# Optimization experiments

Measured on AMD Instinct MI355X. Metric: run time of the kernel, lower is better.

Reference implementation:

```python
import jax, jax.numpy as jnp
import numpy as np

VOL = (256, 256, 256)
K = 64  # number of connected components (clusters)


def setup_inputs() -> dict:
    key = jax.random.key(0)
    k1, k2, k3 = jax.random.split(key, 3)
    # Precomputed connected-component labels of (pred + target) > 0.
    # 0 = background, 1..K = clusters.
    labels = jax.random.randint(k1, VOL, 0, K + 1, dtype=jnp.int32)
    fg = labels > 0
    # Binary prediction / ground-truth masks, nonzero only inside labeled regions
    # (consistent with labels being components of the overlay of pred and target).
    pred = ((jax.random.uniform(k2, VOL) < 0.6) & fg).astype(jnp.float32)
    target = ((jax.random.uniform(k3, VOL) < 0.6) & fg).astype(jnp.float32)
    return {"pred": pred, "target": target, "labels": labels, "num_clusters": K}


def reference(pred, target, labels, num_clusters):
    # Per-cluster dice via one fused segment reduction instead of a Python loop
    # over clusters. Segment 0 is background and is dropped, matching
    # range(1, num_features + 1) in the original.
    lab = labels.reshape(-1)
    p = pred.reshape(-1)
    t = target.reshape(-1)
    nseg = num_clusters + 1
    # intersection = sum(pred_cluster * gt_cluster); pred/target are binary so
    # logical_and(...).float() products reduce to pred * target per segment.
    inter = jax.ops.segment_sum(p * t, lab, num_segments=nseg)[1:]
    sum_p = jax.ops.segment_sum(p, lab, num_segments=nseg)[1:]
    sum_t = jax.ops.segment_sum(t, lab, num_segments=nseg)[1:]
    union = sum_p + sum_t
    dice = jnp.where(union > 0, 2.0 * inter / jnp.maximum(union, 1.0), 1.0)
    return 1.0 - jnp.mean(dice)
```

## Files before the change

kernel.cpp:

```cpp
#include <hip/hip_runtime.h>


#define NSEG 65
#define NREP 64
#define REP_MASK 63
#define NCOPY 16
#define BLOCKS 4096
#define THREADS 256
#define GP 4

__device__ __forceinline__ unsigned int pack32(float p, float t) {
    unsigned int sp = (p != 0.0f) ? 1u : 0u;
    unsigned int st = (t != 0.0f) ? 1u : 0u;
    return ((sp & st) << 20) | (sp << 10) | st;
}

__device__ __forceinline__ void accum4(unsigned int (*s_cnt)[NSEG], int copy,
                                       float4 p, float4 t, int4 l) {
    atomicAdd(&s_cnt[copy][l.x], pack32(p.x, t.x));
    atomicAdd(&s_cnt[copy][l.y], pack32(p.y, t.y));
    atomicAdd(&s_cnt[copy][l.z], pack32(p.z, t.z));
    atomicAdd(&s_cnt[copy][l.w], pack32(p.w, t.w));
}

__global__ __launch_bounds__(THREADS, 8) void seg_count_kernel(
    const float* __restrict__ pred,
    const float* __restrict__ target,
    const int* __restrict__ labels,
    unsigned long long* __restrict__ part,
    int n)
{
    __shared__ unsigned int s_cnt[NCOPY][NSEG];
    const int tid = threadIdx.x;
    const int copy = tid >> 4;
    const int rep = (int)blockIdx.x & REP_MASK;

    for (int i = tid; i < NCOPY * NSEG; i += THREADS)
        ((unsigned int*)s_cnt)[i] = 0u;
    __syncthreads();

    const int n_vec = n >> 2;
    const float4* __restrict__ p4 = (const float4*)pred;
    const float4* __restrict__ t4 = (const float4*)target;
    const int4*   __restrict__ l4 = (const int4*)labels;

    const int chunk = (n_vec + (int)gridDim.x - 1) / (int)gridDim.x;
    const int base = blockIdx.x * chunk;
    const int end = min(base + chunk, n_vec);

    if (end - base == GP * THREADS) {
        int idx = base + tid;
        float4 pa = p4[idx];
        float4 ta = t4[idx];
        int4   la = l4[idx];
        #pragma unroll
        for (int g = 1; g < GP; ++g) {
            float4 pb = p4[idx + g * THREADS];
            float4 tb = t4[idx + g * THREADS];
            int4   lb = l4[idx + g * THREADS];
            accum4(s_cnt, copy, pa, ta, la);
            pa = pb; ta = tb; la = lb;
        }
        accum4(s_cnt, copy, pa, ta, la);
    } else {
        for (int idx = base + tid; idx < end; idx += THREADS)
            accum4(s_cnt, copy, p4[idx], t4[idx], l4[idx]);
    }

    if (blockIdx.x == 0) {
        for (int i = (n_vec << 2) + tid; i < n; i += THREADS)
            atomicAdd(&s_cnt[copy][labels[i]], pack32(pred[i], target[i]));
    }
    __syncthreads();

    for (int s = tid; s < NSEG; s += THREADS) {
        unsigned long long in = 0, sp = 0, st = 0;
        #pragma unroll
        for (int c = 0; c < NCOPY; ++c) {
            unsigned int v = s_cnt[c][s];
            st += v & 0x3FFu;
            sp += (v >> 10) & 0x3FFu;
            in += v >> 20;
        }
        unsigned long long tot = (in << 42) | (sp << 21) | st;
        if (tot) atomicAdd(&part[s * NREP + rep], tot);
    }
}

__global__ __launch_bounds__(256) void dice_finalize_kernel(
    const unsigned long long* __restrict__ part,
    const int* __restrict__ nc_ptr,
    float* __restrict__ out)
{
    const int nc = *nc_ptr;
    const int tid = threadIdx.x;
    const int s = 1 + (tid >> 2);
    const int q = tid & 3;

    unsigned long long acc = 0;
    const unsigned long long* row = part + s * NREP + q * 16;
    #pragma unroll
    for (int i = 0; i < 16; ++i) acc += row[i];
    acc += __shfl_xor(acc, 1);
    acc += __shfl_xor(acc, 2);

    __shared__ float s_dice[64];
    if (q == 0) {
        float in = (float)(acc >> 42);
        float sp = (float)((acc >> 21) & 0x1FFFFFull);
        float st = (float)(acc & 0x1FFFFFull);
        float uni = sp + st;
        float dice = (uni > 0.0f) ? (2.0f * in / uni) : 1.0f;
        s_dice[s - 1] = (s <= nc) ? dice : 0.0f;
    }
    __syncthreads();

    if (tid < 64) {
        float local = s_dice[tid];
        #pragma unroll
        for (int off = 32; off > 0; off >>= 1)
            local += __shfl_down(local, off);
        if (tid == 0) out[0] = 1.0f - local / (float)nc;
    }
}

extern "C" void kernel_launch(void* const* d_in, const int* in_sizes, int n_in,
                              void* d_out, int out_size, void* d_ws, size_t ws_size,
                              hipStream_t stream) {
    const float* pred   = (const float*)d_in[0];
    const float* target = (const float*)d_in[1];
    const int*   labels = (const int*)d_in[2];
    const int*   nc_ptr = (const int*)d_in[3];
    float* out = (float*)d_out;
    unsigned long long* part = (unsigned long long*)d_ws;

    const int n = in_sizes[0];

    hipMemsetAsync(d_ws, 0, NSEG * NREP * sizeof(unsigned long long), stream);

    seg_count_kernel<<<BLOCKS, THREADS, 0, stream>>>(
        pred, target, labels, part, n);
    dice_finalize_kernel<<<1, 256, 0, stream>>>(part, nc_ptr, out);
}
```

Baseline: 200.5 us.

## Software-pipeline loads with inline asm and staggered vmcnt waits, halve grid

Halves the grid and doubles the per-block work to eight float4 groups per thread. The compiler-scheduled loads are replaced with hand-written global_load_dwordx4 asm and explicit s_waitcnt vmcnt counters, so several loads of labels, target and pred stay in flight while LDS atomics run on earlier data. This is meant to hide memory latency better, at the cost of more registers and a lower occupancy hint. The hand-managed wait counts depend on exact issue order and rely on the compiler not inserting other vector-memory ops in between.

New measurement: 200.3 us. No clear change (-0.1%).

```diff
diff --git a/kernel.cpp b/kernel.cpp
--- a/kernel.cpp
+++ b/kernel.cpp
@@ -5,9 +5,21 @@
 #define NREP 64
 #define REP_MASK 63
 #define NCOPY 16
-#define BLOCKS 4096
+#define BLOCKS 2048
 #define THREADS 256
-#define GP 4
+#define GP 8
+
+typedef float4 f4;
+typedef int4 i4;
+
+#define GLOAD(dst, voff, base) \
+    asm volatile("global_load_dwordx4 %0, %1, %2" \
+                 : "=v"(dst) : "v"(voff), "s"(base))
+
+#define WAITN(NSTR) do { \
+    asm volatile("s_waitcnt vmcnt(" NSTR ")" ::: "memory"); \
+    __builtin_amdgcn_sched_barrier(0); \
+} while (0)
 
 __device__ __forceinline__ unsigned int pack32(float p, float t) {
     unsigned int sp = (p != 0.0f) ? 1u : 0u;
@@ -16,14 +28,14 @@
 }
 
 __device__ __forceinline__ void accum4(unsigned int (*s_cnt)[NSEG], int copy,
-                                       float4 p, float4 t, int4 l) {
+                                       f4 p, f4 t, i4 l) {
     atomicAdd(&s_cnt[copy][l.x], pack32(p.x, t.x));
     atomicAdd(&s_cnt[copy][l.y], pack32(p.y, t.y));
     atomicAdd(&s_cnt[copy][l.z], pack32(p.z, t.z));
     atomicAdd(&s_cnt[copy][l.w], pack32(p.w, t.w));
 }
 
-__global__ __launch_bounds__(THREADS, 8) void seg_count_kernel(
+__global__ __launch_bounds__(THREADS, 4) void seg_count_kernel(
     const float* __restrict__ pred,
     const float* __restrict__ target,
     const int* __restrict__ labels,
@@ -40,29 +52,53 @@
     __syncthreads();
 
     const int n_vec = n >> 2;
-    const float4* __restrict__ p4 = (const float4*)pred;
-    const float4* __restrict__ t4 = (const float4*)target;
-    const int4*   __restrict__ l4 = (const int4*)labels;
-
     const int chunk = (n_vec + (int)gridDim.x - 1) / (int)gridDim.x;
     const int base = blockIdx.x * chunk;
     const int end = min(base + chunk, n_vec);
 
     if (end - base == GP * THREADS) {
-        int idx = base + tid;
-        float4 pa = p4[idx];
-        float4 ta = t4[idx];
-        int4   la = l4[idx];
-        #pragma unroll
-        for (int g = 1; g < GP; ++g) {
-            float4 pb = p4[idx + g * THREADS];
-            float4 tb = t4[idx + g * THREADS];
-            int4   lb = l4[idx + g * THREADS];
-            accum4(s_cnt, copy, pa, ta, la);
-            pa = pb; ta = tb; la = lb;
-        }
-        accum4(s_cnt, copy, pa, ta, la);
+        const unsigned int vb = (unsigned int)(base + tid) * 16u;
+        f4 PA, PB;
+        f4 TA, TB, TC;
+        i4 LA, LB, LC, LD;
+
+        GLOAD(LA, vb,           labels);
+        GLOAD(LB, vb + 4096u,   labels);
+        GLOAD(TA, vb,           target);
+        GLOAD(LC, vb + 8192u,   labels);
+        GLOAD(TB, vb + 4096u,   target);
+        GLOAD(PA, vb,           pred);
+
+        GLOAD(LD, vb + 12288u,  labels);
+        GLOAD(TC, vb + 8192u,   target);
+        GLOAD(PB, vb + 4096u,   pred);
+        WAITN("3");  accum4(s_cnt, copy, PA, TA, LA);
+        GLOAD(LA, vb + 16384u,  labels);
+        GLOAD(TA, vb + 12288u,  target);
+        GLOAD(PA, vb + 8192u,   pred);
+        WAITN("3");  accum4(s_cnt, copy, PB, TB, LB);
+        GLOAD(LB, vb + 20480u,  labels);
+        GLOAD(TB, vb + 16384u,  target);
+        GLOAD(PB, vb + 12288u,  pred);
+        WAITN("3");  accum4(s_cnt, copy, PA, TC, LC);
+        GLOAD(LC, vb + 24576u,  labels);
+        GLOAD(TC, vb + 20480u,  target);
+        GLOAD(PA, vb + 16384u,  pred);
+        WAITN("3");  accum4(s_cnt, copy, PB, TA, LD);
+        GLOAD(LD, vb + 28672u,  labels);
+        GLOAD(TA, vb + 24576u,  target);
+        GLOAD(PB, vb + 20480u,  pred);
+        WAITN("3");  accum4(s_cnt, copy, PA, TB, LA);
+        GLOAD(TB, vb + 28672u,  target);
+        GLOAD(PA, vb + 24576u,  pred);
+        WAITN("2");  accum4(s_cnt, copy, PB, TC, LB);
+        GLOAD(PB, vb + 28672u,  pred);
+        WAITN("1");  accum4(s_cnt, copy, PA, TA, LC);
+        WAITN("0");  accum4(s_cnt, copy, PB, TB, LD);
     } else {
+        const f4* __restrict__ p4 = (const f4*)pred;
+        const f4* __restrict__ t4 = (const f4*)target;
+        const i4* __restrict__ l4 = (const i4*)labels;
         for (int idx = base + tid; idx < end; idx += THREADS)
             accum4(s_cnt, copy, p4[idx], t4[idx], l4[idx]);
     }
```
